# Kernel tuning notes

Hardware: AMD Instinct MI355X
Metric: run time of the kernel (lower is better)

## Reference

```python
import jax, jax.numpy as jnp
import numpy as np

NEG = 16        # opt.negative_samples
K_PRED = 6      # opt.subcloud_cube_size - 2
B, C, D = 32, 256, 8
EPS = 1e-11


def _term(z, c, ignore, Wk, dim, k, skip, key):
    # one (dim, k) InfoNCE term
    ax = dim + 2                      # spatial axis in z/c
    s = k + skip
    L = z.shape[ax]
    z_sl = jax.lax.slice_in_dim(z, s, L, axis=ax)        # [B,C,d',h',w']
    c_sl = jax.lax.slice_in_dim(c, 0, L - s, axis=ax)    # [B,C,d',h',w']
    ig = (jax.lax.slice_in_dim(ignore, 0, L - s, axis=dim + 1)
          + jax.lax.slice_in_dim(ignore, s, L, axis=dim + 1))  # [B,d',h',w']

    # 1x1x1 Conv3d (no bias) == channel matmul
    ztwk = jnp.einsum('bcdhw,oc->dhwbo', z_sl, Wk)       # [d,h,w,B,O]
    d, h, w, b, o = ztwk.shape
    M = d * h * w * b
    flat = ztwk.reshape(M, o)
    # random negative sampling: same row index replicated across channels
    idx = jax.random.randint(key, (M * NEG,), 0, M)
    shuf = flat[idx].reshape(d, h, w, b, NEG, o)          # [d,h,w,B,N,O]

    ctx = jnp.transpose(c_sl, (2, 3, 4, 0, 1))            # [d,h,w,B,C]
    main = jnp.einsum('dhwbc,dhwbc->dhwb', ctx, ztwk)     # positive score
    negs = jnp.einsum('dhwbc,dhwbnc->dhwbn', ctx, shuf)   # negative scores
    scores = jnp.concatenate([main[..., None], negs], axis=-1)  # [d,h,w,B,1+N]

    probs = jax.nn.softmax(scores, axis=-1)
    logp0 = jnp.log(probs[..., 0] + EPS)                  # [d,h,w,B]
    nll = -jnp.transpose(logp0, (3, 0, 1, 2))             # [B,d,h,w]
    mask = (ig == 0)
    # NLL with target 0 everywhere, ignore_index on masked-out positions, mean reduction
    return (nll * mask).sum() / mask.sum()


def setup_inputs() -> dict:
    key = jax.random.key(0)
    kz, kc, kt, kw = jax.random.split(key, 4)
    z = jax.random.normal(kz, (B, C, D, D, D), dtype=jnp.float32)
    c = jax.random.normal(kc, (B, C, D, D, D), dtype=jnp.float32)
    targets_to_ignore = jax.random.randint(kt, (B, D, D, D), 0, 2, dtype=jnp.int32)
    Wk = jax.random.normal(kw, (K_PRED, C, C), dtype=jnp.float32) * 0.02  # [K,O,C]
    return {"z": z, "c": c, "targets_to_ignore": targets_to_ignore,
            "Wk": Wk, "skip_step": 1}


def reference(z, c, targets_to_ignore, Wk, skip_step):
    keys = jax.random.split(jax.random.key(42), 3 * K_PRED)
    total = jnp.float32(0.0)
    i = 0
    for dim in range(3):
        for k in range(1, K_PRED + 1):
            total = total + _term(z, c, targets_to_ignore, Wk[k - 1],
                                  dim, k, skip_step, keys[i])
            i += 1
    return total / (3 * K_PRED)
```

## Files before the change

kernel.cpp:

```cpp
#include <hip/hip_runtime.h>
#include <stdint.h>

#define EPSL 1e-11f

typedef _Float16 h2 __attribute__((ext_vector_type(2)));
typedef _Float16 h8 __attribute__((ext_vector_type(8)));
typedef __attribute__((ext_vector_type(4))) float f32x4;
typedef __attribute__((ext_vector_type(16))) float f32x16;

__device__ __forceinline__ uint32_t pk2h(float a, float b) {
    union { h2 h; uint32_t u; } t;
    t.h = (h2){ (_Float16)a, (_Float16)b };
    return t.u;
}
__device__ __forceinline__ uint16_t f2h(float a) {
    union { _Float16 h; uint16_t u; } t; t.h = (_Float16)a; return t.u;
}

__device__ __forceinline__ uint64_t sm64(uint64_t x) {
    x += 0x9E3779B97F4A7C15ULL;
    x = (x ^ (x >> 30)) * 0xBF58476D1CE4E5B9ULL;
    x = (x ^ (x >> 27)) * 0x94D049BB133111EBULL;
    return x ^ (x >> 31);
}

__device__ __forceinline__ uint32_t rowz_of(uint32_t f, int dim, int S, int s) {
    uint32_t b = f & 31u;
    uint32_t r = f >> 5;
    uint32_t d, h, w;
    if (dim == 0) {
        w = r & 7u; h = (r >> 3) & 7u; d = (r >> 6) + (uint32_t)s;
    } else if (dim == 1) {
        w = r & 7u; uint32_t q = r >> 3;
        h = q % (uint32_t)S + (uint32_t)s; d = q / (uint32_t)S;
    } else {
        w = r % (uint32_t)S + (uint32_t)s; uint32_t q = r / (uint32_t)S;
        h = q & 7u; d = q >> 3;
    }
    return b * 512u + d * 64u + h * 8u + w;
}


__global__ __launch_bounds__(256) void k_prepall(const float* __restrict__ z,
                                                 const float* __restrict__ c,
                                                 const float* __restrict__ W,
                                                 uint16_t* __restrict__ zh,
                                                 uint16_t* __restrict__ cTh,
                                                 uint16_t* __restrict__ Whf,
                                                 float* sums_s, int* cnts_s) {
    const int bid = blockIdx.x;
    const int t = threadIdx.x;
    if (bid < 4096) {
        __shared__ float tile[32][65];
        const int zz = bid >> 6;
        const int b = zz & 31, isC = zz >> 5;
        const float* src = (isC ? c : z) + (size_t)b * 131072;
        const int p0 = (bid & 7) * 64, ch0 = ((bid >> 3) & 7) * 32;
        const int pl = t & 63, cl0 = t >> 6;
        #pragma unroll
        for (int i = 0; i < 8; i++)
            tile[cl0 + i * 4][pl] = src[(ch0 + cl0 + i * 4) * 512 + p0 + pl];
        __syncthreads();
        const int ml = t >> 2, ck = (t & 3) * 8;
        uint4 o;
        o.x = pk2h(tile[ck + 0][ml], tile[ck + 1][ml]);
        o.y = pk2h(tile[ck + 2][ml], tile[ck + 3][ml]);
        o.z = pk2h(tile[ck + 4][ml], tile[ck + 5][ml]);
        o.w = pk2h(tile[ck + 6][ml], tile[ck + 7][ml]);
        uint16_t* dst = isC ? cTh : zh;
        *(uint4*)(dst + (size_t)(b * 512 + p0 + ml) * 256 + ch0 + ck) = o;
    } else if (bid < 4288) {
        const int gid = (bid - 4096) * 4 + (t >> 6);
        const int lane = t & 63;
        const int kk = gid >> 7, rem = gid & 127;
        const int ks2 = rem >> 3, ot = rem & 7;
        const int o = ot * 32 + (lane & 31);
        const int cc = ks2 * 16 + (lane >> 5) * 8;
        const float* src = W + ((size_t)kk * 256 + o) * 256 + cc;
        float4 v0 = *(const float4*)src;
        float4 v1 = *(const float4*)(src + 4);
        uint4 out = make_uint4(pk2h(v0.x, v0.y), pk2h(v0.z, v0.w),
                               pk2h(v1.x, v1.y), pk2h(v1.z, v1.w));
        *(uint4*)(Whf + (size_t)gid * 512 + lane * 8) = out;
    } else {
        int t2 = (bid - 4288) * 256 + t;
        if (t2 < 1152) { sums_s[t2] = 0.f; cnts_s[t2] = 0; }
    }
}

__global__ __launch_bounds__(256, 2) void k_gemm(const uint16_t* __restrict__ zh,
                                                 const uint16_t* __restrict__ Whf,
                                                 uint16_t* __restrict__ ZWh) {
    __shared__ __align__(16) uint16_t smem[16384];
    const int kk = blockIdx.y;
    const int t = threadIdx.x, lane = t & 63, wv = t >> 6;
    const int m0 = blockIdx.x * 128 + wv * 32;
    const int col = lane & 31, hl = lane >> 5;
    const uint16_t* W32 = Whf + (size_t)kk * 65536;
    const uint16_t* A0 = zh + (size_t)(m0 + col) * 256 + hl * 8;

    f32x16 acc[8];
    #pragma unroll
    for (int i = 0; i < 8; i++)
        #pragma unroll
        for (int jj = 0; jj < 16; jj++) acc[i][jj] = 0.f;

    #define BSTAGE(sk_, buf_) { \
        const char* gb_ = (const char*)W32 + (size_t)(sk_) * 16384 + wv * 4096 + lane * 16; \
        char* lb_ = (char*)smem + (buf_) * 16384 + wv * 4096; \
        _Pragma("unroll") \
        for (int i_ = 0; i_ < 4; i_++) \
            __builtin_amdgcn_global_load_lds( \
                (const __attribute__((address_space(1))) void*)(gb_ + i_ * 1024), \
                (__attribute__((address_space(3))) void*)(lb_ + i_ * 1024), 16, 0, 0); \
    }

    BSTAGE(0, 0);
    asm volatile("s_waitcnt vmcnt(0)" ::: "memory");
    __syncthreads();
    for (int sk = 0; sk < 8; sk++) {
        if (sk < 7) BSTAGE(sk + 1, (sk + 1) & 1);
        const uint16_t* Bb = smem + (sk & 1) * 8192;
        #pragma unroll
        for (int half = 0; half < 2; half++) {
            h8 a = *(const h8*)(A0 + (sk * 2 + half) * 16);
            const uint16_t* Bh = Bb + half * 4096;
            #pragma unroll
            for (int ot = 0; ot < 8; ot++) {
                h8 bv = *(const h8*)(&Bh[ot * 512 + lane * 8]);
                acc[ot] = __builtin_amdgcn_mfma_f32_32x32x16_f16(a, bv, acc[ot], 0, 0, 0);
            }
        }
        asm volatile("s_waitcnt vmcnt(0)" ::: "memory");
        __syncthreads();
    }
    #undef BSTAGE

    uint16_t* Lb = smem + wv * 4096;
    uint16_t* dstbase = ZWh + ((size_t)kk * 16384 + m0) * 256;
    #pragma unroll
    for (int hh = 0; hh < 2; hh++) {
        #pragma unroll
        for (int ot = 0; ot < 8; ot++)
            #pragma unroll
            for (int rg = 0; rg < 8; rg++) {
                int reg = hh * 8 + rg;
                int row = (reg & 3) + 8 * (reg >> 2) + 4 * hl;
                Lb[(row - hh * 16) * 256 + ot * 32 + col] = f2h(acc[ot][reg]);
            }
        const uint4* Lr = (const uint4*)Lb;
        uint4* dst = (uint4*)(dstbase + hh * 16 * 256);
        #pragma unroll
        for (int i = 0; i < 8; i++)
            dst[i * 64 + lane] = Lr[i * 64 + lane];
    }
}

__global__ __launch_bounds__(256, 4) void k_score(const uint16_t* __restrict__ ZWh,
                                                  const uint16_t* __restrict__ cTh,
                                                  const int* __restrict__ ign,
                                                  float* sums_s, int* cnts_s) {
    __shared__ float sbuf[4][288];
    __shared__ float wsum[4], wcnt[4];
    int bid = blockIdx.x;
    int kk = 0, cum = 0;
    for (;;) { int nb = 96 * (6 - kk); if (bid < cum + nb) break; cum += nb; kk++; }
    const int S = 6 - kk, T = S * 2048, s = kk + 2;
    const uint16_t* ZW = ZWh + (size_t)kk * 16384 * 256;

    const int local = bid - cum;
    const int dim = local / (32 * S);
    const int loc2 = local - dim * 32 * S;
    const int term = dim * 6 + kk;

    const int t = threadIdx.x, lane = t & 63, wv = t >> 6;
    const int lm = lane & 15, lq = lane >> 4;
    const uint32_t gidx = (uint32_t)(loc2 * 4 + wv);
    const uint32_t b = gidx & 31u;
    const uint32_t rb = gidx >> 5;
    const uint32_t r = rb * 16u + (uint32_t)lm;

    uint32_t d, h, w;
    if (dim == 0)      { w = r & 7u; h = (r >> 3) & 7u; d = r >> 6; }
    else if (dim == 1) { w = r & 7u; uint32_t qq = r >> 3; h = qq % (uint32_t)S; d = qq / (uint32_t)S; }
    else               { w = r % (uint32_t)S; uint32_t qq = r / (uint32_t)S; h = qq & 7u; d = qq >> 3; }
    uint32_t pc = d * 64u + h * 8u + w;
    uint32_t pz = pc + (dim == 0 ? (uint32_t)s * 64u : dim == 1 ? (uint32_t)s * 8u : (uint32_t)s);
    uint32_t rowc = b * 512u + pc;
    uint32_t rowz = b * 512u + pz;

    uint64_t x = sm64(((uint64_t)term << 40) +
                      (uint64_t)gidx * 128u + (uint64_t)lm);
    uint32_t nrow = rowz_of((uint32_t)(x >> 32) % (uint32_t)T, dim, S, s);

    int mok = (ign[rowc] + ign[rowz]) == 0;

    const uint16_t* cA = cTh + (size_t)rowc * 256 + lq * 8;
    const uint16_t* pB = ZW + (size_t)rowz * 256 + lq * 8;
    const uint16_t* nB = ZW + (size_t)nrow * 256 + lq * 8;

    h8 af[8], pf[8], nf[8];
    #pragma unroll
    for (int ks = 0; ks < 8; ks++) af[ks] = *(const h8*)(cA + ks * 32);
    #pragma unroll
    for (int ks = 0; ks < 8; ks++) pf[ks] = *(const h8*)(pB + ks * 32);
    #pragma unroll
    for (int ks = 0; ks < 8; ks++) nf[ks] = *(const h8*)(nB + ks * 32);

    f32x4 accp = (f32x4){0.f, 0.f, 0.f, 0.f};
    f32x4 accn = (f32x4){0.f, 0.f, 0.f, 0.f};
    #pragma unroll
    for (int ks = 0; ks < 8; ks++)
        accp = __builtin_amdgcn_mfma_f32_16x16x32_f16(af[ks], pf[ks], accp, 0, 0, 0);
    #pragma unroll
    for (int ks = 0; ks < 8; ks++)
        accn = __builtin_amdgcn_mfma_f32_16x16x32_f16(af[ks], nf[ks], accn, 0, 0, 0);

    float* Sb = sbuf[wv];
    #pragma unroll
    for (int rg = 0; rg < 4; rg++)
        Sb[(lq * 4 + rg) * 17 + lm] = accn[rg];
    if ((lm >> 2) == lq) Sb[272 + lm] = accp[lm & 3];

    float dpos = Sb[272 + lm];
    float mx = dpos;
    float scn[16];
    #pragma unroll
    for (int n = 0; n < 16; n++) { scn[n] = Sb[lm * 17 + n]; mx = fmaxf(mx, scn[n]); }
    float e0 = __expf(dpos - mx), sum = e0;
    #pragma unroll
    for (int n = 0; n < 16; n++) sum += __expf(scn[n] - mx);
    float nll = -__logf(e0 / sum + EPSL);

    float v = mok ? nll : 0.f;
    float cm = mok ? 1.f : 0.f;
    #pragma unroll
    for (int st = 1; st < 64; st <<= 1) {
        v  += __shfl_xor(v, st, 64);
        cm += __shfl_xor(cm, st, 64);
    }
    if (lane == 0) { wsum[wv] = v * 0.25f; wcnt[wv] = cm * 0.25f; }
    __syncthreads();
    if (t == 0) {
        float sv = wsum[0] + wsum[1] + wsum[2] + wsum[3];
        float cv = wcnt[0] + wcnt[1] + wcnt[2] + wcnt[3];
        int slot = blockIdx.x & 63;
        atomicAdd(&sums_s[term * 64 + slot], sv);
        atomicAdd(&cnts_s[term * 64 + slot], (int)(cv + 0.5f));
    }
}

__global__ void k_final(const float* __restrict__ sums_s, const int* __restrict__ cnts_s,
                        float* __restrict__ out) {
    __shared__ float ratio[18];
    int t = threadIdx.x;
    if (t < 18) {
        float sv = 0.f; int cv = 0;
        #pragma unroll 8
        for (int i = 0; i < 64; i++) { sv += sums_s[t * 64 + i]; cv += cnts_s[t * 64 + i]; }
        ratio[t] = sv / (float)cv;
    }
    __syncthreads();
    if (t == 0) {
        float tot = 0.f;
        #pragma unroll
        for (int i = 0; i < 18; i++) tot += ratio[i];
        out[0] = tot / 18.f;
    }
}

extern "C" void kernel_launch(void* const* d_in, const int* in_sizes, int n_in,
                              void* d_out, int out_size, void* d_ws, size_t ws_size,
                              hipStream_t stream) {
    const float* z   = (const float*)d_in[0];
    const float* c   = (const float*)d_in[1];
    const int*   ign = (const int*)d_in[2];
    const float* Wk  = (const float*)d_in[3];

    float* sums_s = (float*)d_ws;
    int*   cnts_s = (int*)((char*)d_ws + 4608);
    uint16_t* zh  = (uint16_t*)((char*)d_ws + 65536);
    uint16_t* cTh = zh  + (size_t)16384 * 256;
    uint16_t* Whf = cTh + (size_t)16384 * 256;
    uint16_t* ZWh = Whf + (size_t)6 * 65536;

    hipLaunchKernelGGL(k_prepall, dim3(4293), dim3(256), 0, stream,
                       z, c, Wk, zh, cTh, Whf, sums_s, cnts_s);
    hipLaunchKernelGGL(k_gemm, dim3(128, 6), dim3(256), 0, stream, zh, Whf, ZWh);
    hipLaunchKernelGGL(k_score, dim3(2016), dim3(256), 0, stream, ZWh, cTh, ign, sums_s, cnts_s);
    hipLaunchKernelGGL(k_final, dim3(1), dim3(64), 0, stream, sums_s, cnts_s, (float*)d_out);
}
```

Before: 129.0 us.

## Fuse final reduction into score kernel, vectorize prep loads, double GEMM stage depth

The separate final-reduction launch is removed: the last k_score block, found with an atomic ticket counter, sums the per-term partials and writes the output. The prep kernel now reads z/c with float4 loads instead of scalar loads. The GEMM streams 32 KB of W per stage over 4 iterations instead of 16 KB over 8, which halves the barriers but doubles LDS use and may limit occupancy. The ticket is reset in the prep kernel.

```diff
diff --git a/kernel.cpp b/kernel.cpp
--- a/kernel.cpp
+++ b/kernel.cpp
@@ -56,10 +56,14 @@
         const int b = zz & 31, isC = zz >> 5;
         const float* src = (isC ? c : z) + (size_t)b * 131072;
         const int p0 = (bid & 7) * 64, ch0 = ((bid >> 3) & 7) * 32;
-        const int pl = t & 63, cl0 = t >> 6;
-        #pragma unroll
-        for (int i = 0; i < 8; i++)
-            tile[cl0 + i * 4][pl] = src[(ch0 + cl0 + i * 4) * 512 + p0 + pl];
+        #pragma unroll
+        for (int it = 0; it < 2; it++) {
+            int f = t + it * 256;
+            int chv = f >> 4, p4 = (f & 15) * 4;
+            float4 v = *(const float4*)(src + (size_t)(ch0 + chv) * 512 + p0 + p4);
+            tile[chv][p4 + 0] = v.x; tile[chv][p4 + 1] = v.y;
+            tile[chv][p4 + 2] = v.z; tile[chv][p4 + 3] = v.w;
+        }
         __syncthreads();
         const int ml = t >> 2, ck = (t & 3) * 8;
         uint4 o;
@@ -84,14 +88,17 @@
         *(uint4*)(Whf + (size_t)gid * 512 + lane * 8) = out;
     } else {
         int t2 = (bid - 4288) * 256 + t;
-        if (t2 < 1152) { sums_s[t2] = 0.f; cnts_s[t2] = 0; }
+        if (t2 < 1153) {
+            if (t2 < 1152) sums_s[t2] = 0.f;
+            cnts_s[t2] = 0;
+        }
     }
 }
 
 __global__ __launch_bounds__(256, 2) void k_gemm(const uint16_t* __restrict__ zh,
                                                  const uint16_t* __restrict__ Whf,
                                                  uint16_t* __restrict__ ZWh) {
-    __shared__ __align__(16) uint16_t smem[16384];
+    __shared__ __align__(16) uint16_t smem[32768];
     const int kk = blockIdx.y;
     const int t = threadIdx.x, lane = t & 63, wv = t >> 6;
     const int m0 = blockIdx.x * 128 + wv * 32;
@@ -106,10 +113,10 @@
         for (int jj = 0; jj < 16; jj++) acc[i][jj] = 0.f;
 
     #define BSTAGE(sk_, buf_) { \
-        const char* gb_ = (const char*)W32 + (size_t)(sk_) * 16384 + wv * 4096 + lane * 16; \
-        char* lb_ = (char*)smem + (buf_) * 16384 + wv * 4096; \
+        const char* gb_ = (const char*)W32 + (size_t)(sk_) * 32768 + wv * 8192 + lane * 16; \
+        char* lb_ = (char*)smem + (buf_) * 32768 + wv * 8192; \
         _Pragma("unroll") \
-        for (int i_ = 0; i_ < 4; i_++) \
+        for (int i_ = 0; i_ < 8; i_++) \
             __builtin_amdgcn_global_load_lds( \
                 (const __attribute__((address_space(1))) void*)(gb_ + i_ * 1024), \
                 (__attribute__((address_space(3))) void*)(lb_ + i_ * 1024), 16, 0, 0); \
@@ -118,12 +125,12 @@
     BSTAGE(0, 0);
     asm volatile("s_waitcnt vmcnt(0)" ::: "memory");
     __syncthreads();
-    for (int sk = 0; sk < 8; sk++) {
-        if (sk < 7) BSTAGE(sk + 1, (sk + 1) & 1);
-        const uint16_t* Bb = smem + (sk & 1) * 8192;
-        #pragma unroll
-        for (int half = 0; half < 2; half++) {
-            h8 a = *(const h8*)(A0 + (sk * 2 + half) * 16);
+    for (int sk = 0; sk < 4; sk++) {
+        if (sk < 3) BSTAGE(sk + 1, (sk + 1) & 1);
+        const uint16_t* Bb = smem + (sk & 1) * 16384;
+        #pragma unroll
+        for (int half = 0; half < 4; half++) {
+            h8 a = *(const h8*)(A0 + (sk * 4 + half) * 16);
             const uint16_t* Bh = Bb + half * 4096;
             #pragma unroll
             for (int ot = 0; ot < 8; ot++) {
@@ -159,9 +166,11 @@
 __global__ __launch_bounds__(256, 4) void k_score(const uint16_t* __restrict__ ZWh,
                                                   const uint16_t* __restrict__ cTh,
                                                   const int* __restrict__ ign,
-                                                  float* sums_s, int* cnts_s) {
+                                                  float* sums_s, int* cnts_s,
+                                                  int* ticket, float* out) {
     __shared__ float sbuf[4][288];
     __shared__ float wsum[4], wcnt[4];
+    __shared__ int isLast;
     int bid = blockIdx.x;
     int kk = 0, cum = 0;
     for (;;) { int nb = 96 * (6 - kk); if (bid < cum + nb) break; cum += nb; kk++; }
@@ -247,25 +256,29 @@
         int slot = blockIdx.x & 63;
         atomicAdd(&sums_s[term * 64 + slot], sv);
         atomicAdd(&cnts_s[term * 64 + slot], (int)(cv + 0.5f));
-    }
-}
-
-__global__ void k_final(const float* __restrict__ sums_s, const int* __restrict__ cnts_s,
-                        float* __restrict__ out) {
-    __shared__ float ratio[18];
-    int t = threadIdx.x;
-    if (t < 18) {
-        float sv = 0.f; int cv = 0;
-        #pragma unroll 8
-        for (int i = 0; i < 64; i++) { sv += sums_s[t * 64 + i]; cv += cnts_s[t * 64 + i]; }
-        ratio[t] = sv / (float)cv;
+        __threadfence();
+        int done = atomicAdd(ticket, 1);
+        isLast = (done == 2015);
     }
     __syncthreads();
-    if (t == 0) {
-        float tot = 0.f;
-        #pragma unroll
-        for (int i = 0; i < 18; i++) tot += ratio[i];
-        out[0] = tot / 18.f;
+    if (isLast) {
+        __shared__ float ratio[18];
+        if (t < 18) {
+            float sv = 0.f; int cv = 0;
+            #pragma unroll 8
+            for (int i = 0; i < 64; i++) {
+                sv += atomicAdd(&sums_s[t * 64 + i], 0.f);
+                cv += atomicAdd(&cnts_s[t * 64 + i], 0);
+            }
+            ratio[t] = sv / (float)cv;
+        }
+        __syncthreads();
+        if (t == 0) {
+            float tot = 0.f;
+            #pragma unroll
+            for (int i = 0; i < 18; i++) tot += ratio[i];
+            out[0] = tot / 18.f;
+        }
     }
 }
 
@@ -279,6 +292,7 @@
 
     float* sums_s = (float*)d_ws;
     int*   cnts_s = (int*)((char*)d_ws + 4608);
+    int*   ticket = cnts_s + 1152;
     uint16_t* zh  = (uint16_t*)((char*)d_ws + 65536);
     uint16_t* cTh = zh  + (size_t)16384 * 256;
     uint16_t* Whf = cTh + (size_t)16384 * 256;
@@ -287,6 +301,6 @@
     hipLaunchKernelGGL(k_prepall, dim3(4293), dim3(256), 0, stream,
                        z, c, Wk, zh, cTh, Whf, sums_s, cnts_s);
     hipLaunchKernelGGL(k_gemm, dim3(128, 6), dim3(256), 0, stream, zh, Whf, ZWh);
-    hipLaunchKernelGGL(k_score, dim3(2016), dim3(256), 0, stream, ZWh, cTh, ign, sums_s, cnts_s);
-    hipLaunchKernelGGL(k_final, dim3(1), dim3(64), 0, stream, sums_s, cnts_s, (float*)d_out);
-}
+    hipLaunchKernelGGL(k_score, dim3(2016), dim3(256), 0, stream,
+                       ZWh, cTh, ign, sums_s, cnts_s, ticket, (float*)d_out);
+}
```

After: 195.6 us. 51.6% more time.
